# Kernel tuning notes

Hardware: AMD Instinct MI355X
Metric: run time of the kernel (lower is better)

The kernel has to match this reference:

```python
import jax, jax.numpy as jnp
import numpy as np

BN_EPS = 1e-5


def setup_inputs() -> dict:
    key = jax.random.key(0)
    ks = jax.random.split(key, 10)
    B, C, Ci, H, W = 4, 256, 128, 64, 64
    s = 0.05
    return {
        "x": jax.random.normal(ks[0], (B, C, H, W), jnp.float32),
        "g_w": jax.random.normal(ks[1], (Ci, C), jnp.float32) * s,
        "g_b": jax.random.normal(ks[2], (Ci,), jnp.float32) * s,
        "theta_w": jax.random.normal(ks[3], (Ci, C), jnp.float32) * s,
        "theta_b": jax.random.normal(ks[4], (Ci,), jnp.float32) * s,
        "phi_w": jax.random.normal(ks[5], (Ci, C), jnp.float32) * s,
        "phi_b": jax.random.normal(ks[6], (Ci,), jnp.float32) * s,
        "W_w": jax.random.normal(ks[7], (C, Ci), jnp.float32) * s,
        "W_b": jax.random.normal(ks[8], (C,), jnp.float32) * s,
        "bn_gamma": jnp.ones((C,), jnp.float32),
        "bn_beta": jnp.zeros((C,), jnp.float32),
        "scale": jax.random.normal(ks[9], (1,), jnp.float32),
    }


def reference(x, g_w, g_b, theta_w, theta_b, phi_w, phi_b, W_w, W_b, bn_gamma, bn_beta, scale):
    B, C, H, W = x.shape
    xf = x.reshape(B, C, H * W)  # [B, C, N]
    # 1x1 conv projections == channel matmuls
    g = jnp.einsum('oc,bcn->bno', g_w, xf) + g_b            # [B, N, Ci]
    th = jnp.einsum('oc,bcn->bno', theta_w, xf) + theta_b   # [B, N, Ci]
    ph = jnp.einsum('oc,bcn->bon', phi_w, xf) + phi_b[:, None]  # [B, Ci, N]
    # unscaled attention: f = theta @ phi, softmax over keys
    f = jnp.einsum('bnd,bdm->bnm', th, ph)                  # [B, N, N]
    attn = jax.nn.softmax(f, axis=-1)
    y = jnp.einsum('bnm,bmo->bno', attn, g)                 # [B, N, Ci]
    y4 = y.transpose(0, 2, 1).reshape(B, -1, H, W)          # [B, Ci, H, W]
    # W: 1x1 conv + BatchNorm2d (training mode: batch statistics)
    wy = jnp.einsum('od,bdhw->bohw', W_w, y4) + W_b[None, :, None, None]
    mean = wy.mean(axis=(0, 2, 3))
    var = wy.var(axis=(0, 2, 3))
    bn = (wy - mean[None, :, None, None]) * jax.lax.rsqrt(var[None, :, None, None] + BN_EPS)
    bn = bn * bn_gamma[None, :, None, None] + bn_beta[None, :, None, None]
    return scale * bn + x
```

## Files before the change

kernel.cpp:

```cpp
#include <hip/hip_runtime.h>
#include <hip/hip_bf16.h>

#define BB 4
#define CC 256
#define CI 128
#define NN 4096

typedef _Float16 f16;
typedef __attribute__((ext_vector_type(8))) _Float16 f16x8;
typedef __attribute__((ext_vector_type(4))) float f32x4;

#define MFMA(a,b,c) __builtin_amdgcn_mfma_f32_16x16x32_f16(a,b,c,0,0,0)
#define LDS3(p) ((__attribute__((address_space(3))) void*)(p))
#define GL1(p)  ((const __attribute__((address_space(1))) void*)(p))

#define DPP_MAX(x, ctrl) { int _s=__float_as_int(x); \
    float _y=__int_as_float(__builtin_amdgcn_update_dpp(_s,_s,ctrl,0xF,0xF,false)); \
    x = fmaxf(x,_y); }
#define DPP_ADD(x, ctrl) { int _s=__float_as_int(x); \
    float _y=__int_as_float(__builtin_amdgcn_update_dpp(_s,_s,ctrl,0xF,0xF,false)); \
    x = x+_y; }
__device__ __forceinline__ float rowmax16(float x){
    DPP_MAX(x,0xB1) DPP_MAX(x,0x4E) DPP_MAX(x,0x141) DPP_MAX(x,0x140) return x;
}
__device__ __forceinline__ float rowsum16(float x){
    DPP_ADD(x,0xB1) DPP_ADD(x,0x4E) DPP_ADD(x,0x141) DPP_ADD(x,0x140) return x;
}

__global__ __launch_bounds__(256) void k0_cast(const float* tw, const float* pw,
                                               const float* gw, const float* Ww, f16* dst){
    int i = blockIdx.x*256 + threadIdx.x;
    int j = i & 32767; int sel = i >> 15;
    const float* s = (sel==0)? tw : (sel==1)? pw : (sel==2)? gw : Ww;
    dst[i] = (f16)s[j];
}

__global__ __launch_bounds__(256) void k1_xpose(const float* x, f16* xt){
    int nt = blockIdx.x, ct = blockIdx.y, b = blockIdx.z;
    __shared__ float tile[64][65];
    int t = threadIdx.x;
    const float* src = x + ((size_t)(b*CC + ct*64))*NN + nt*64;
    #pragma unroll
    for (int k=0;k<16;k++){ int idx=t+k*256; int cl=idx>>6, nl=idx&63;
        tile[cl][nl]=src[(size_t)cl*NN + nl]; }
    __syncthreads();
    f16* dst = xt + ((size_t)(b*NN + nt*64))*CC + ct*64;
    #pragma unroll
    for (int k=0;k<16;k++){ int idx=t+k*256; int nl=idx>>6, cl=idx&63;
        dst[(size_t)nl*CC + cl] = (f16)tile[cl][nl]; }
}

__global__ __launch_bounds__(256) void k2a_proj(const f16* xt, const f16* thw, const f16* phw,
                                                const float* thb, const float* phb,
                                                f16* th, f16* ph){
    int b = blockIdx.y; int ntile = blockIdx.x; int mat = blockIdx.z;
    int wv = threadIdx.x>>6, lane = threadIdx.x&63, q=lane>>4, cc=lane&15;
    int n0 = ntile*128 + wv*32;
    f16x8 aq[2][8];
    #pragma unroll
    for (int ns=0;ns<2;ns++){
        const f16* ap = xt + ((size_t)(b*NN + n0 + ns*16 + cc))*CC + q*8;
        #pragma unroll
        for (int kk=0;kk<8;kk++) aq[ns][kk] = *(const f16x8*)(ap + kk*32);
    }
    const f16* w   = mat? phw : thw;
    const float* bias = mat? phb : thb;
    f16* o = mat? ph : th;
    #pragma unroll 1
    for (int os=0;os<8;os++){
        f32x4 acc0={0,0,0,0}, acc1={0,0,0,0};
        const f16* wp = w + ((size_t)(os*16 + cc))*CC + q*8;
        #pragma unroll
        for (int kk=0;kk<8;kk++){
            f16x8 bf = *(const f16x8*)(wp + kk*32);
            acc0 = MFMA(aq[0][kk], bf, acc0);
            acc1 = MFMA(aq[1][kk], bf, acc1);
        }
        float bv = bias[os*16+cc];
        #pragma unroll
        for (int r=0;r<4;r++){
            o[((size_t)(b*NN + n0      + 4*q + r))*CI + os*16 + cc] = (f16)(acc0[r] + bv);
            o[((size_t)(b*NN + n0 + 16 + 4*q + r))*CI + os*16 + cc] = (f16)(acc1[r] + bv);
        }
    }
}

__global__ __launch_bounds__(256) void k2b_g(const f16* xt, const f16* gwh, const float* gb, f16* gt2){
    int b = blockIdx.y; int mt = blockIdx.x;
    int wv=threadIdx.x>>6, lane=threadIdx.x&63, q=lane>>4, cc=lane&15;
    f16x8 ag[2][8];
    #pragma unroll
    for (int os=0;os<2;os++){
        const f16* ap = gwh + ((size_t)(wv*32 + os*16 + cc))*CC + q*8;
        #pragma unroll
        for (int kk=0;kk<8;kk++) ag[os][kk] = *(const f16x8*)(ap + kk*32);
    }
    f32x4 acc[2][4];
    #pragma unroll
    for (int os=0;os<2;os++){
        #pragma unroll
        for (int ms=0;ms<4;ms++) acc[os][ms]=(f32x4){0,0,0,0};
    }
    #pragma unroll 1
    for (int kk=0;kk<8;kk++){
        #pragma unroll
        for (int ms=0;ms<4;ms++){
            f16x8 bf = *(const f16x8*)(xt + ((size_t)(b*NN + mt*64 + ms*16 + cc))*CC + kk*32 + q*8);
            acc[0][ms]=MFMA(ag[0][kk],bf,acc[0][ms]);
            acc[1][ms]=MFMA(ag[1][kk],bf,acc[1][ms]);
        }
    }
    #pragma unroll
    for (int os=0;os<2;os++){
        #pragma unroll
        for (int r=0;r<4;r++){
            int orow = wv*32 + os*16 + 4*q + r;
            float bv = gb[orow];
            #pragma unroll
            for (int ms=0;ms<4;ms++)
                gt2[((size_t)(b*64 + mt))*8192 + orow*64 + ms*16 + cc] = (f16)(acc[os][ms][r] + bv);
        }
    }
}

__global__ __launch_bounds__(256, 2) void k3_attn(const f16* th, const f16* ph, const f16* gt2,
                                                  f16* ypart, float* ml){
    int qt = blockIdx.x;
    int sp = blockIdx.y;
    int b  = blockIdx.z;
    int wv=threadIdx.x>>6, lane=threadIdx.x&63, q=lane>>4, cc=lane&15;
    int qrow0 = qt*128 + wv*32;
    int kv0 = sp*1024;
    int sw  = (cc&7)<<4;

    __shared__ __align__(16) char ldsb[81920];
    char* phL = ldsb;
    char* gtL = ldsb + 32768;
    char* plw = ldsb + 65536 + wv*4096;

    f16x8 aq[2][4];
    #pragma unroll
    for (int rb=0;rb<2;rb++){
        const f16* thp = th + ((size_t)(b*NN + qrow0 + rb*16 + cc))*CI + q*8;
        #pragma unroll
        for (int kk=0;kk<4;kk++) aq[rb][kk] = *(const f16x8*)(thp + kk*32);
    }

    const char* phg = (const char*)(ph + (size_t)b*NN*CI);
    int ph_row = wv*16 + (lane>>4);
    int ph_c   = (lane&15)*16;
    const char* gtg = (const char*)gt2 + (size_t)b*64*16384;
    int gt_flat = wv*4096 + lane*16;

    f32x4 yacc[2][8];
    #pragma unroll
    for (int rb=0;rb<2;rb++)
        #pragma unroll
        for (int os=0;os<8;os++) yacc[rb][os]=(f32x4){0,0,0,0};
    float m_run[2][4];
    f32x4 l_vec[2];
    #pragma unroll
    for (int rb=0;rb<2;rb++){
        l_vec[rb]=(f32x4){0,0,0,0};
        #pragma unroll
        for (int r=0;r<4;r++) m_run[rb][r]=-1e30f;
    }

    {
        char* pbase = phL + wv*4096;
        char* gbase = gtL + wv*4096;
        #pragma unroll
        for (int ch=0; ch<4; ch++){
            int prow = ph_row + ch*4;
            const char* ps = phg + (size_t)(kv0 + prow)*256 + (ph_c ^ ((prow&7)<<4));
            __builtin_amdgcn_global_load_lds(GL1(ps), LDS3(pbase + ch*1024), 16, 0, 0);
            int gf = gt_flat + ch*1024;
            int grow = gf >> 7;
            const char* gs = gtg + (size_t)(sp*16)*16384 + grow*128 + ((gf&127) ^ ((grow&7)<<4));
            __builtin_amdgcn_global_load_lds(GL1(gs), LDS3(gbase + ch*1024), 16, 0, 0);
        }
    }
    __syncthreads();

    int cur = 0;
    #pragma unroll 1
    for (int it=0; it<16; ++it){
        if (it < 15){
            int m0n = kv0 + (it+1)*64;
            char* pbase = phL + (cur^1)*16384 + wv*4096;
            char* gbase = gtL + (cur^1)*16384 + wv*4096;
            #pragma unroll
            for (int ch=0; ch<4; ch++){
                int prow = ph_row + ch*4;
                const char* ps = phg + (size_t)(m0n + prow)*256 + (ph_c ^ ((prow&7)<<4));
                __builtin_amdgcn_global_load_lds(GL1(ps), LDS3(pbase + ch*1024), 16, 0, 0);
                int gf = gt_flat + ch*1024;
                int grow = gf >> 7;
                const char* gs = gtg + (size_t)(sp*16 + it+1)*16384 + grow*128 + ((gf&127) ^ ((grow&7)<<4));
                __builtin_amdgcn_global_load_lds(GL1(gs), LDS3(gbase + ch*1024), 16, 0, 0);
            }
        }
        const char* pt  = phL + cur*16384;
        const char* gtt = gtL + cur*16384;
        f32x4 fa[2][4];
        #pragma unroll
        for (int j=0;j<4;j++){
            f16x8 pf[4];
            #pragma unroll
            for (int kk=0;kk<4;kk++)
                pf[kk] = *(const f16x8*)(pt + (j*16+cc)*256 + ((kk*64 + q*16) ^ sw));
            fa[0][j]=(f32x4){0,0,0,0}; fa[1][j]=(f32x4){0,0,0,0};
            #pragma unroll
            for (int kk=0;kk<4;kk++){
                fa[0][j]=MFMA(aq[0][kk], pf[kk], fa[0][j]);
                fa[1][j]=MFMA(aq[1][kk], pf[kk], fa[1][j]);
            }
        }
        float mx[2][4]; float need = 0.f;
        #pragma unroll
        for (int rb=0;rb<2;rb++){
            #pragma unroll
            for (int r=0;r<4;r++){
                float m0 = fmaxf(fmaxf(fa[rb][0][r],fa[rb][1][r]), fmaxf(fa[rb][2][r],fa[rb][3][r]));
                m0 = rowmax16(m0);
                mx[rb][r]=m0;
                need = fmaxf(need, m0 - m_run[rb][r]);
            }
        }
        if (__any(need > 3.f)){
            #pragma unroll
            for (int rb=0;rb<2;rb++){
                #pragma unroll
                for (int r=0;r<4;r++){
                    float nm = fmaxf(m_run[rb][r], mx[rb][r]);
                    float co = __expf(m_run[rb][r]-nm);
                    m_run[rb][r]=nm;
                    l_vec[rb][r]*=co;
                    #pragma unroll
                    for (int os=0;os<8;os++) yacc[rb][os][r]*=co;
                }
            }
        }
        #pragma unroll
        for (int rb=0;rb<2;rb++){
            #pragma unroll
            for (int j=0;j<4;j++){
                #pragma unroll
                for (int r=0;r<4;r++) fa[rb][j][r]=__expf(fa[rb][j][r]-m_run[rb][r]);
            }
            #pragma unroll
            for (int r=0;r<4;r++)
                l_vec[rb][r] += (fa[rb][0][r]+fa[rb][1][r]) + (fa[rb][2][r]+fa[rb][3][r]);
        }
        #pragma unroll
        for (int rb=0;rb<2;rb++){
            #pragma unroll
            for (int j=0;j<4;j++){
                #pragma unroll
                for (int r=0;r<4;r++){
                    *(f16*)(plw + (rb*16+4*q+r)*128 + (((j*16+cc)*2) ^ (((4*q+r)&7)<<4))) = (f16)fa[rb][j][r];
                }
            }
        }
        #pragma unroll
        for (int kk2=0;kk2<2;kk2++){
            f16x8 pa0 = *(const f16x8*)(plw +  cc     *128 + ((q*16 + kk2*64) ^ sw));
            f16x8 pa1 = *(const f16x8*)(plw + (16+cc) *128 + ((q*16 + kk2*64) ^ sw));
            #pragma unroll
            for (int os=0;os<8;os++){
                f16x8 gv = *(const f16x8*)(gtt + (os*16+cc)*128 + ((kk2*64 + q*16) ^ sw));
                yacc[0][os] = MFMA(pa0, gv, yacc[0][os]);
                yacc[1][os] = MFMA(pa1, gv, yacc[1][os]);
            }
        }
        __syncthreads();
        cur ^= 1;
    }
    float linv[2][4], lred[2][4];
    #pragma unroll
    for (int rb=0;rb<2;rb++)
        #pragma unroll
        for (int r=0;r<4;r++){
            float l = rowsum16(l_vec[rb][r]);
            lred[rb][r]=l; linv[rb][r]=1.f/l;
        }
    #pragma unroll
    for (int rb=0;rb<2;rb++){
        #pragma unroll
        for (int os=0;os<8;os++){
            #pragma unroll
            for (int r=0;r<4;r++)
                ypart[((size_t)((sp*4+b)*NN + qrow0 + rb*16 + 4*q + r))*CI + os*16 + cc] = (f16)(yacc[rb][os][r]*linv[rb][r]);
        }
    }
    if (cc==0){
        #pragma unroll
        for (int rb=0;rb<2;rb++){
            #pragma unroll
            for (int r=0;r<4;r++){
                size_t row = (size_t)(sp*4+b)*NN + qrow0 + rb*16 + 4*q + r;
                ml[row*2]   = m_run[rb][r];
                ml[row*2+1] = lred[rb][r];
            }
        }
    }
}

__global__ __launch_bounds__(256) void k3c(const f16* ypart, const float* ml,
                                           f16* y, float* part, float* mupart){
    int blk = blockIdx.x; int t = threadIdx.x;
    int rloc = t>>2;
    int row  = blk*64 + rloc;
    int b = row>>12, n = row & 4095;
    int o0 = (t&3)*32;
    __shared__ __align__(16) f16 ldsT[128*64];
    float m_s[4], l_s[4];
    #pragma unroll
    for (int s=0;s<4;s++){ size_t r2 = ((size_t)(s*4+b)*NN + n)*2; m_s[s]=ml[r2]; l_s[s]=ml[r2+1]; }
    float M = fmaxf(fmaxf(m_s[0],m_s[1]),fmaxf(m_s[2],m_s[3]));
    float w[4]; float L=0.f;
    #pragma unroll
    for (int s=0;s<4;s++){ w[s]=l_s[s]*__expf(m_s[s]-M); L+=w[s]; }
    float inv = 1.f/L;
    #pragma unroll
    for (int s=0;s<4;s++) w[s]*=inv;
    float acc[32];
    #pragma unroll
    for (int j=0;j<32;j++) acc[j]=0.f;
    #pragma unroll
    for (int s=0;s<4;s++){
        const f16* src = ypart + ((size_t)(s*4+b)*NN + n)*CI + o0;
        #pragma unroll
        for (int v=0;v<4;v++){
            f16x8 vv = *(const f16x8*)(src + v*8);
            #pragma unroll
            for (int e=0;e<8;e++) acc[v*8+e] += w[s]*(float)vv[e];
        }
    }
    f16* yo = y + (size_t)row*CI + o0;
    #pragma unroll
    for (int v=0;v<4;v++){
        f16x8 ov;
        #pragma unroll
        for (int e=0;e<8;e++) ov[e] = (f16)acc[v*8+e];
        *(f16x8*)(yo + v*8) = ov;
        #pragma unroll
        for (int e=0;e<8;e++){
            int o = o0 + v*8 + e;
            ldsT[o*64 + (rloc ^ ((o&7)<<3))] = ov[e];
        }
    }
    __syncthreads();
    int wv=t>>6, lane=t&63, q=lane>>4, cc=lane&15;
    f32x4 gacc[2][8];
    #pragma unroll
    for (int a=0;a<2;a++)
        #pragma unroll
        for (int c2=0;c2<8;c2++) gacc[a][c2]=(f32x4){0,0,0,0};
    f16x8 af[2][2];
    #pragma unroll
    for (int o1t=0;o1t<2;o1t++){
        int o1 = (wv*2+o1t)*16+cc;
        #pragma unroll
        for (int kk=0;kk<2;kk++)
            af[o1t][kk] = *(const f16x8*)(ldsT + o1*64 + ((kk*32+q*8) ^ ((o1&7)<<3)));
    }
    #pragma unroll 1
    for (int o2t=0;o2t<8;o2t++){
        int o2 = o2t*16+cc;
        #pragma unroll
        for (int kk=0;kk<2;kk++){
            f16x8 bf = *(const f16x8*)(ldsT + o2*64 + ((kk*32+q*8) ^ ((o2&7)<<3)));
            gacc[0][o2t] = MFMA(af[0][kk], bf, gacc[0][o2t]);
            gacc[1][o2t] = MFMA(af[1][kk], bf, gacc[1][o2t]);
        }
    }
    float* pb = part + (size_t)blk*16384;
    #pragma unroll
    for (int o1t=0;o1t<2;o1t++){
        #pragma unroll
        for (int o2t=0;o2t<8;o2t++){
            #pragma unroll
            for (int r=0;r<4;r++)
                pb[((wv*2+o1t)*16+4*q+r)*128 + o2t*16+cc] = gacc[o1t][o2t][r];
        }
    }
    if (t<128){
        float sm=0.f;
        #pragma unroll
        for (int v=0;v<8;v++){
            f16x8 vv = *(const f16x8*)(ldsT + t*64 + ((v*8) ^ ((t&7)<<3)));
            #pragma unroll
            for (int e=0;e<8;e++) sm += (float)vv[e];
        }
        mupart[blk*128 + t] = sm;
    }
}

__global__ __launch_bounds__(256) void k4b_red(const float* part, const float* mupart, float* S){
    int pc = blockIdx.y;
    int t = threadIdx.x;
    if (blockIdx.x < 64){
        int i = blockIdx.x*256 + t;
        float s=0.f;
        #pragma unroll 1
        for (int p=pc*32; p<pc*32+32; p++) s += part[(size_t)p*16384 + i];
        atomicAdd(&S[i], s);
    } else if (t < 128){
        float s=0.f;
        #pragma unroll 1
        for (int p=pc*32; p<pc*32+32; p++) s += mupart[p*128 + t];
        atomicAdd(&S[16384+t], s);
    }
}

__global__ __launch_bounds__(128) void k4c_coef(const float* S, const float* Ww, const float* Wb,
                                                const float* gamma, const float* beta,
                                                const float* scale, float* AB){
    int ch = blockIdx.x; int t = threadIdx.x;
    const float* w = Ww + ch*CI;
    float tmp=0.f;
    const float* Srow = S + t*CI;
    #pragma unroll 1
    for (int o2=0;o2<CI;o2++) tmp += Srow[o2]*w[o2];
    float v  = w[t]*tmp;
    float mc = w[t]*S[16384 + t];
    #pragma unroll
    for (int s=1;s<64;s<<=1){ v += __shfl_xor(v,s); mc += __shfl_xor(mc,s); }
    __shared__ float red[4];
    if ((t&63)==0){ red[(t>>6)*2]=v; red[(t>>6)*2+1]=mc; }
    __syncthreads();
    if (t==0){
        float wSw = red[0]+red[2];
        float wmu = red[1]+red[3];
        const float M = 16384.f;
        float meanwy = wmu/M + Wb[ch];
        float var = wSw/M - (wmu/M)*(wmu/M);
        float inv = rsqrtf(var + 1e-5f);
        float sc = scale[0];
        float A  = sc*gamma[ch]*inv;
        float B3 = sc*(beta[ch] - meanwy*inv*gamma[ch]);
        AB[ch]     = A;
        AB[256+ch] = B3 + A*Wb[ch];
    }
}

__global__ __launch_bounds__(256) void k5_out(const f16* Wwh, const f16* y, const float* x,
                                              const float* AB, float* out){
    int ntile = blockIdx.x;
    int cht   = blockIdx.y;
    int b     = blockIdx.z;
    int wv=threadIdx.x>>6, lane=threadIdx.x&63, q=lane>>4, cc=lane&15;
    int ch0 = cht*64 + wv*16;
    f16x8 aw[4];
    const f16* wp = Wwh + ((size_t)(ch0+cc))*CI + q*8;
    #pragma unroll
    for (int kk=0;kk<4;kk++) aw[kk]=*(const f16x8*)(wp+kk*32);
    float Ar[4], Br[4];
    #pragma unroll
    for (int r=0;r<4;r++){ Ar[r]=AB[ch0+4*q+r]; Br[r]=AB[256+ch0+4*q+r]; }
    #pragma unroll 1
    for (int ns=0;ns<16;ns++){
        int n0 = ntile*256 + ns*16;
        f32x4 acc={0,0,0,0};
        const f16* yp = y + ((size_t)(b*NN + n0 + cc))*CI + q*8;
        #pragma unroll
        for (int kk=0;kk<4;kk++) acc = MFMA(aw[kk], *(const f16x8*)(yp+kk*32), acc);
        #pragma unroll
        for (int r=0;r<4;r++){
            size_t addr = ((size_t)(b*CC + ch0 + 4*q + r))*NN + n0 + cc;
            out[addr] = x[addr] + Ar[r]*acc[r] + Br[r];
        }
    }
}

extern "C" void kernel_launch(void* const* d_in, const int* in_sizes, int n_in,
                              void* d_out, int out_size, void* d_ws, size_t ws_size,
                              hipStream_t stream){
    const float* x    = (const float*)d_in[0];
    const float* g_w  = (const float*)d_in[1];
    const float* g_b  = (const float*)d_in[2];
    const float* th_w = (const float*)d_in[3];
    const float* th_b = (const float*)d_in[4];
    const float* ph_w = (const float*)d_in[5];
    const float* ph_b = (const float*)d_in[6];
    const float* W_w  = (const float*)d_in[7];
    const float* W_b  = (const float*)d_in[8];
    const float* bg   = (const float*)d_in[9];
    const float* bb   = (const float*)d_in[10];
    const float* sc   = (const float*)d_in[11];

    char* ws = (char*)d_ws;
    f16* xt  = (f16*)(ws);
    f16* th  = (f16*)(ws + 8388608);
    f16* ph  = (f16*)(ws + 8388608 + 1*4194304);
    f16* gt2 = (f16*)(ws + 8388608 + 2*4194304);
    f16* y   = (f16*)(ws + 8388608 + 3*4194304);
    f16* wh  = (f16*)(ws + 8388608 + 4*4194304);
    float* ml    = (float*)(ws + 25427968);
    f16*   ypart = (f16*)(ws + 25952256);
    float* mupart= (float*)(ws + 42729472);
    float* part  = (float*)ws;
    float* S    = (float*)(ws + 42860544);
    float* AB   = (float*)(ws + 42926592);
    f16* th_wh = wh;
    f16* ph_wh = wh + 32768;
    f16* g_wh  = wh + 65536;
    f16* Ww_h  = wh + 98304;

    hipMemsetAsync(S, 0, 16512*sizeof(float), stream);
    hipLaunchKernelGGL(k0_cast,  dim3(512),     dim3(256), 0, stream, th_w, ph_w, g_w, W_w, wh);
    hipLaunchKernelGGL(k1_xpose, dim3(64,4,4),  dim3(256), 0, stream, x, xt);
    hipLaunchKernelGGL(k2a_proj, dim3(32,4,2),  dim3(256), 0, stream, xt, th_wh, ph_wh, th_b, ph_b, th, ph);
    hipLaunchKernelGGL(k2b_g,    dim3(64,4),    dim3(256), 0, stream, xt, g_wh, g_b, gt2);
    hipLaunchKernelGGL(k3_attn,  dim3(32,4,4),  dim3(256), 0, stream, th, ph, gt2, ypart, ml);
    hipLaunchKernelGGL(k3c,      dim3(256),     dim3(256), 0, stream, ypart, ml, y, part, mupart);
    hipLaunchKernelGGL(k4b_red,  dim3(65,8),    dim3(256), 0, stream, part, mupart, S);
    hipLaunchKernelGGL(k4c_coef, dim3(256),     dim3(128), 0, stream, S, W_w, W_b, bg, bb, sc, AB);
    hipLaunchKernelGGL(k5_out,   dim3(16,4,4),  dim3(256), 0, stream, Ww_h, y, x, AB, (float*)d_out);
}
```

Measured before the change: 164.6 us.

## Merge cast/transpose and projection kernels, halve attention KV tile for occupancy

Folds the weight-cast kernel into the transpose kernel and merges the theta/phi and g projection kernels into one launch, removing two kernel launches. The attention kernel now stages 32-key tiles instead of 64, halving LDS use (80KB to 40KB) and requesting 3 blocks per CU, with new swizzle patterns for the narrower rows. The output kernel uses twice as many blocks with half the work each. The smaller KV tile doubles the loop iterations and the barrier count in attention, which may cancel the gain from higher occupancy.

```diff
diff --git a/kernel.cpp b/kernel.cpp
--- a/kernel.cpp
+++ b/kernel.cpp
@@ -27,15 +27,9 @@
     DPP_ADD(x,0xB1) DPP_ADD(x,0x4E) DPP_ADD(x,0x141) DPP_ADD(x,0x140) return x;
 }
 
-__global__ __launch_bounds__(256) void k0_cast(const float* tw, const float* pw,
-                                               const float* gw, const float* Ww, f16* dst){
-    int i = blockIdx.x*256 + threadIdx.x;
-    int j = i & 32767; int sel = i >> 15;
-    const float* s = (sel==0)? tw : (sel==1)? pw : (sel==2)? gw : Ww;
-    dst[i] = (f16)s[j];
-}
-
-__global__ __launch_bounds__(256) void k1_xpose(const float* x, f16* xt){
+__global__ __launch_bounds__(256) void k01_xpose(const float* x, f16* xt,
+                                                 const float* tw, const float* pw,
+                                                 const float* gw, const float* Ww, f16* wdst){
     int nt = blockIdx.x, ct = blockIdx.y, b = blockIdx.z;
     __shared__ float tile[64][65];
     int t = threadIdx.x;
@@ -48,82 +42,89 @@
     #pragma unroll
     for (int k=0;k<16;k++){ int idx=t+k*256; int nl=idx>>6, cl=idx&63;
         dst[(size_t)nl*CC + cl] = (f16)tile[cl][nl]; }
-}
-
-__global__ __launch_bounds__(256) void k2a_proj(const f16* xt, const f16* thw, const f16* phw,
-                                                const float* thb, const float* phb,
-                                                f16* th, f16* ph){
-    int b = blockIdx.y; int ntile = blockIdx.x; int mat = blockIdx.z;
+    if (t < 128){
+        int blkId = blockIdx.x + 64*(blockIdx.y + 4*blockIdx.z);
+        int i = blkId*128 + t;
+        int j = i & 32767; int sel = i >> 15;
+        const float* s = (sel==0)? tw : (sel==1)? pw : (sel==2)? gw : Ww;
+        wdst[i] = (f16)s[j];
+    }
+}
+
+__global__ __launch_bounds__(256) void k2_all(const f16* xt, const f16* thw, const f16* phw,
+                                              const f16* gwh, const float* thb, const float* phb,
+                                              const float* gb, f16* th, f16* ph, f16* gt2){
+    int b = blockIdx.y; int xx = blockIdx.x;
     int wv = threadIdx.x>>6, lane = threadIdx.x&63, q=lane>>4, cc=lane&15;
-    int n0 = ntile*128 + wv*32;
-    f16x8 aq[2][8];
-    #pragma unroll
-    for (int ns=0;ns<2;ns++){
-        const f16* ap = xt + ((size_t)(b*NN + n0 + ns*16 + cc))*CC + q*8;
-        #pragma unroll
-        for (int kk=0;kk<8;kk++) aq[ns][kk] = *(const f16x8*)(ap + kk*32);
-    }
-    const f16* w   = mat? phw : thw;
-    const float* bias = mat? phb : thb;
-    f16* o = mat? ph : th;
-    #pragma unroll 1
-    for (int os=0;os<8;os++){
-        f32x4 acc0={0,0,0,0}, acc1={0,0,0,0};
-        const f16* wp = w + ((size_t)(os*16 + cc))*CC + q*8;
-        #pragma unroll
+    if (xx < 64){
+        int mat = xx>>5; int ntile = xx&31;
+        int n0 = ntile*128 + wv*32;
+        f16x8 aq[2][8];
+        #pragma unroll
+        for (int ns=0;ns<2;ns++){
+            const f16* ap = xt + ((size_t)(b*NN + n0 + ns*16 + cc))*CC + q*8;
+            #pragma unroll
+            for (int kk=0;kk<8;kk++) aq[ns][kk] = *(const f16x8*)(ap + kk*32);
+        }
+        const f16* w   = mat? phw : thw;
+        const float* bias = mat? phb : thb;
+        f16* o = mat? ph : th;
+        #pragma unroll 1
+        for (int os=0;os<8;os++){
+            f32x4 acc0={0,0,0,0}, acc1={0,0,0,0};
+            const f16* wp = w + ((size_t)(os*16 + cc))*CC + q*8;
+            #pragma unroll
+            for (int kk=0;kk<8;kk++){
+                f16x8 bf = *(const f16x8*)(wp + kk*32);
+                acc0 = MFMA(aq[0][kk], bf, acc0);
+                acc1 = MFMA(aq[1][kk], bf, acc1);
+            }
+            float bv = bias[os*16+cc];
+            #pragma unroll
+            for (int r=0;r<4;r++){
+                o[((size_t)(b*NN + n0      + 4*q + r))*CI + os*16 + cc] = (f16)(acc0[r] + bv);
+                o[((size_t)(b*NN + n0 + 16 + 4*q + r))*CI + os*16 + cc] = (f16)(acc1[r] + bv);
+            }
+        }
+    } else {
+        int mt = xx - 64;
+        f16x8 ag[2][8];
+        #pragma unroll
+        for (int os=0;os<2;os++){
+            const f16* ap = gwh + ((size_t)(wv*32 + os*16 + cc))*CC + q*8;
+            #pragma unroll
+            for (int kk=0;kk<8;kk++) ag[os][kk] = *(const f16x8*)(ap + kk*32);
+        }
+        f32x4 acc[2][4];
+        #pragma unroll
+        for (int os=0;os<2;os++){
+            #pragma unroll
+            for (int ms=0;ms<4;ms++) acc[os][ms]=(f32x4){0,0,0,0};
+        }
+        #pragma unroll 1
         for (int kk=0;kk<8;kk++){
-            f16x8 bf = *(const f16x8*)(wp + kk*32);
-            acc0 = MFMA(aq[0][kk], bf, acc0);
-            acc1 = MFMA(aq[1][kk], bf, acc1);
-        }
-        float bv = bias[os*16+cc];
-        #pragma unroll
-        for (int r=0;r<4;r++){
-            o[((size_t)(b*NN + n0      + 4*q + r))*CI + os*16 + cc] = (f16)(acc0[r] + bv);
-            o[((size_t)(b*NN + n0 + 16 + 4*q + r))*CI + os*16 + cc] = (f16)(acc1[r] + bv);
-        }
-    }
-}
-
-__global__ __launch_bounds__(256) void k2b_g(const f16* xt, const f16* gwh, const float* gb, f16* gt2){
-    int b = blockIdx.y; int mt = blockIdx.x;
-    int wv=threadIdx.x>>6, lane=threadIdx.x&63, q=lane>>4, cc=lane&15;
-    f16x8 ag[2][8];
-    #pragma unroll
-    for (int os=0;os<2;os++){
-        const f16* ap = gwh + ((size_t)(wv*32 + os*16 + cc))*CC + q*8;
-        #pragma unroll
-        for (int kk=0;kk<8;kk++) ag[os][kk] = *(const f16x8*)(ap + kk*32);
-    }
-    f32x4 acc[2][4];
-    #pragma unroll
-    for (int os=0;os<2;os++){
-        #pragma unroll
-        for (int ms=0;ms<4;ms++) acc[os][ms]=(f32x4){0,0,0,0};
-    }
-    #pragma unroll 1
-    for (int kk=0;kk<8;kk++){
-        #pragma unroll
-        for (int ms=0;ms<4;ms++){
-            f16x8 bf = *(const f16x8*)(xt + ((size_t)(b*NN + mt*64 + ms*16 + cc))*CC + kk*32 + q*8);
-            acc[0][ms]=MFMA(ag[0][kk],bf,acc[0][ms]);
-            acc[1][ms]=MFMA(ag[1][kk],bf,acc[1][ms]);
-        }
-    }
-    #pragma unroll
-    for (int os=0;os<2;os++){
-        #pragma unroll
-        for (int r=0;r<4;r++){
-            int orow = wv*32 + os*16 + 4*q + r;
-            float bv = gb[orow];
-            #pragma unroll
-            for (int ms=0;ms<4;ms++)
-                gt2[((size_t)(b*64 + mt))*8192 + orow*64 + ms*16 + cc] = (f16)(acc[os][ms][r] + bv);
-        }
-    }
-}
-
-__global__ __launch_bounds__(256, 2) void k3_attn(const f16* th, const f16* ph, const f16* gt2,
+            #pragma unroll
+            for (int ms=0;ms<4;ms++){
+                f16x8 bf = *(const f16x8*)(xt + ((size_t)(b*NN + mt*64 + ms*16 + cc))*CC + kk*32 + q*8);
+                acc[0][ms]=MFMA(ag[0][kk],bf,acc[0][ms]);
+                acc[1][ms]=MFMA(ag[1][kk],bf,acc[1][ms]);
+            }
+        }
+        #pragma unroll
+        for (int os=0;os<2;os++){
+            #pragma unroll
+            for (int r=0;r<4;r++){
+                int orow = wv*32 + os*16 + 4*q + r;
+                float bv = gb[orow];
+                #pragma unroll
+                for (int ms=0;ms<4;ms++)
+                    gt2[((size_t)(b*64 + mt))*8192 + orow*64 + ms*16 + cc] = (f16)(acc[os][ms][r] + bv);
+            }
+        }
+    }
+}
+
+__global__ __launch_bounds__(256, 3) void k3_attn(const f16* th, const f16* ph, const f16* gt2,
                                                   f16* ypart, float* ml){
     int qt = blockIdx.x;
     int sp = blockIdx.y;
@@ -132,11 +133,12 @@
     int qrow0 = qt*128 + wv*32;
     int kv0 = sp*1024;
     int sw  = (cc&7)<<4;
-
-    __shared__ __align__(16) char ldsb[81920];
+    int sw2 = ((cc>>1)&3)<<4;
+
+    __shared__ __align__(16) char ldsb[40960];
     char* phL = ldsb;
-    char* gtL = ldsb + 32768;
-    char* plw = ldsb + 65536 + wv*4096;
+    char* gtL = ldsb + 16384;
+    char* plw = ldsb + 32768 + wv*2048;
 
     f16x8 aq[2][4];
     #pragma unroll
@@ -147,10 +149,7 @@
     }
 
     const char* phg = (const char*)(ph + (size_t)b*NN*CI);
-    int ph_row = wv*16 + (lane>>4);
-    int ph_c   = (lane&15)*16;
     const char* gtg = (const char*)gt2 + (size_t)b*64*16384;
-    int gt_flat = wv*4096 + lane*16;
 
     f32x4 yacc[2][8];
     #pragma unroll
@@ -166,45 +165,36 @@
         for (int r=0;r<4;r++) m_run[rb][r]=-1e30f;
     }
 
-    {
-        char* pbase = phL + wv*4096;
-        char* gbase = gtL + wv*4096;
-        #pragma unroll
-        for (int ch=0; ch<4; ch++){
-            int prow = ph_row + ch*4;
-            const char* ps = phg + (size_t)(kv0 + prow)*256 + (ph_c ^ ((prow&7)<<4));
+    auto STAGE = [&](int tt, int bb){
+        int key0 = kv0 + tt*32;
+        int mt  = key0 >> 6;
+        int kob = (key0 & 32)*2;
+        char* pbase = phL + bb*8192 + wv*2048;
+        char* gbase = gtL + bb*8192 + wv*2048;
+        #pragma unroll
+        for (int ch=0; ch<2; ch++){
+            int prow = wv*8 + ch*4 + (lane>>4);
+            const char* ps = phg + (size_t)(key0 + prow)*256 + (((lane&15)*16) ^ ((prow&7)<<4));
             __builtin_amdgcn_global_load_lds(GL1(ps), LDS3(pbase + ch*1024), 16, 0, 0);
-            int gf = gt_flat + ch*1024;
-            int grow = gf >> 7;
-            const char* gs = gtg + (size_t)(sp*16)*16384 + grow*128 + ((gf&127) ^ ((grow&7)<<4));
+            int gf = wv*2048 + ch*1024 + lane*16;
+            int grow = gf>>6, gcol = gf&63;
+            const char* gs = gtg + (size_t)mt*16384 + grow*128 + kob + (gcol ^ (((grow>>1)&3)<<4));
             __builtin_amdgcn_global_load_lds(GL1(gs), LDS3(gbase + ch*1024), 16, 0, 0);
         }
-    }
+    };
+
+    STAGE(0, 0);
     __syncthreads();
 
     int cur = 0;
     #pragma unroll 1
-    for (int it=0; it<16; ++it){
-        if (it < 15){
-            int m0n = kv0 + (it+1)*64;
-            char* pbase = phL + (cur^1)*16384 + wv*4096;
-            char* gbase = gtL + (cur^1)*16384 + wv*4096;
-            #pragma unroll
-            for (int ch=0; ch<4; ch++){
-                int prow = ph_row + ch*4;
-                const char* ps = phg + (size_t)(m0n + prow)*256 + (ph_c ^ ((prow&7)<<4));
-                __builtin_amdgcn_global_load_lds(GL1(ps), LDS3(pbase + ch*1024), 16, 0, 0);
-                int gf = gt_flat + ch*1024;
-                int grow = gf >> 7;
-                const char* gs = gtg + (size_t)(sp*16 + it+1)*16384 + grow*128 + ((gf&127) ^ ((grow&7)<<4));
-                __builtin_amdgcn_global_load_lds(GL1(gs), LDS3(gbase + ch*1024), 16, 0, 0);
-            }
-        }
-        const char* pt  = phL + cur*16384;
-        const char* gtt = gtL + cur*16384;
-        f32x4 fa[2][4];
-        #pragma unroll
-        for (int j=0;j<4;j++){
+    for (int it=0; it<32; ++it){
+        if (it < 31) STAGE(it+1, cur^1);
+        const char* pt  = phL + cur*8192;
+        const char* gtt = gtL + cur*8192;
+        f32x4 fa[2][2];
+        #pragma unroll
+        for (int j=0;j<2;j++){
             f16x8 pf[4];
             #pragma unroll
             for (int kk=0;kk<4;kk++)
@@ -221,7 +211,7 @@
         for (int rb=0;rb<2;rb++){
             #pragma unroll
             for (int r=0;r<4;r++){
-                float m0 = fmaxf(fmaxf(fa[rb][0][r],fa[rb][1][r]), fmaxf(fa[rb][2][r],fa[rb][3][r]));
+                float m0 = fmaxf(fa[rb][0][r],fa[rb][1][r]);
                 m0 = rowmax16(m0);
                 mx[rb][r]=m0;
                 need = fmaxf(need, m0 - m_run[rb][r]);
@@ -244,31 +234,31 @@
         #pragma unroll
         for (int rb=0;rb<2;rb++){
             #pragma unroll
-            for (int j=0;j<4;j++){
+            for (int j=0;j<2;j++){
                 #pragma unroll
                 for (int r=0;r<4;r++) fa[rb][j][r]=__expf(fa[rb][j][r]-m_run[rb][r]);
             }
             #pragma unroll
             for (int r=0;r<4;r++)
-                l_vec[rb][r] += (fa[rb][0][r]+fa[rb][1][r]) + (fa[rb][2][r]+fa[rb][3][r]);
+                l_vec[rb][r] += fa[rb][0][r]+fa[rb][1][r];
         }
         #pragma unroll
         for (int rb=0;rb<2;rb++){
             #pragma unroll
-            for (int j=0;j<4;j++){
+            for (int j=0;j<2;j++){
                 #pragma unroll
                 for (int r=0;r<4;r++){
-                    *(f16*)(plw + (rb*16+4*q+r)*128 + (((j*16+cc)*2) ^ (((4*q+r)&7)<<4))) = (f16)fa[rb][j][r];
+                    int swp = (((2*q) + (r>>1))&3)<<4;
+                    *(f16*)(plw + (rb*16+4*q+r)*64 + (((j*16+cc)*2) ^ swp)) = (f16)fa[rb][j][r];
                 }
             }
         }
-        #pragma unroll
-        for (int kk2=0;kk2<2;kk2++){
-            f16x8 pa0 = *(const f16x8*)(plw +  cc     *128 + ((q*16 + kk2*64) ^ sw));
-            f16x8 pa1 = *(const f16x8*)(plw + (16+cc) *128 + ((q*16 + kk2*64) ^ sw));
+        {
+            f16x8 pa0 = *(const f16x8*)(plw +  cc     *64 + ((q*16) ^ sw2));
+            f16x8 pa1 = *(const f16x8*)(plw + (16+cc) *64 + ((q*16) ^ sw2));
             #pragma unroll
             for (int os=0;os<8;os++){
-                f16x8 gv = *(const f16x8*)(gtt + (os*16+cc)*128 + ((kk2*64 + q*16) ^ sw));
+                f16x8 gv = *(const f16x8*)(gtt + (os*16+cc)*64 + ((q*16) ^ sw2));
                 yacc[0][os] = MFMA(pa0, gv, yacc[0][os]);
                 yacc[1][os] = MFMA(pa1, gv, yacc[1][os]);
             }
@@ -460,8 +450,8 @@
     #pragma unroll
     for (int r=0;r<4;r++){ Ar[r]=AB[ch0+4*q+r]; Br[r]=AB[256+ch0+4*q+r]; }
     #pragma unroll 1
-    for (int ns=0;ns<16;ns++){
-        int n0 = ntile*256 + ns*16;
+    for (int ns=0;ns<8;ns++){
+        int n0 = ntile*128 + ns*16;
         f32x4 acc={0,0,0,0};
         const f16* yp = y + ((size_t)(b*NN + n0 + cc))*CI + q*8;
         #pragma unroll
@@ -509,13 +499,12 @@
     f16* Ww_h  = wh + 98304;
 
     hipMemsetAsync(S, 0, 16512*sizeof(float), stream);
-    hipLaunchKernelGGL(k0_cast,  dim3(512),     dim3(256), 0, stream, th_w, ph_w, g_w, W_w, wh);
-    hipLaunchKernelGGL(k1_xpose, dim3(64,4,4),  dim3(256), 0, stream, x, xt);
-    hipLaunchKernelGGL(k2a_proj, dim3(32,4,2),  dim3(256), 0, stream, xt, th_wh, ph_wh, th_b, ph_b, th, ph);
-    hipLaunchKernelGGL(k2b_g,    dim3(64,4),    dim3(256), 0, stream, xt, g_wh, g_b, gt2);
+    hipLaunchKernelGGL(k01_xpose, dim3(64,4,4), dim3(256), 0, stream, x, xt, th_w, ph_w, g_w, W_w, wh);
+    hipLaunchKernelGGL(k2_all,   dim3(128,4),   dim3(256), 0, stream, xt, th_wh, ph_wh, g_wh,
+                       th_b, ph_b, g_b, th, ph, gt2);
     hipLaunchKernelGGL(k3_attn,  dim3(32,4,4),  dim3(256), 0, stream, th, ph, gt2, ypart, ml);
     hipLaunchKernelGGL(k3c,      dim3(256),     dim3(256), 0, stream, ypart, ml, y, part, mupart);
     hipLaunchKernelGGL(k4b_red,  dim3(65,8),    dim3(256), 0, stream, part, mupart, S);
     hipLaunchKernelGGL(k4c_coef, dim3(256),     dim3(128), 0, stream, S, W_w, W_b, bg, bb, sc, AB);
-    hipLaunchKernelGGL(k5_out,   dim3(16,4,4),  dim3(256), 0, stream, Ww_h, y, x, AB, (float*)d_out);
-}
+    hipLaunchKernelGGL(k5_out,   dim3(32,4,4),  dim3(256), 0, stream, Ww_h, y, x, AB, (float*)d_out);
+}
```

Measured after the change: 169.2 us. +2.8%, slower.
